# Kernel tuning notes

Hardware: AMD Instinct MI355X
Metric: run time of the kernel (lower is better)

Reference implementation:

```python
import jax, jax.numpy as jnp
import numpy as np

DIM = 1024
HEADS = 16
HEAD_DIM = DIM // HEADS
HIDDEN = 4096
EPS = 1e-5


def _layer_norm(x, w, b):
    mu = jnp.mean(x, axis=-1, keepdims=True)
    var = jnp.var(x, axis=-1, keepdims=True)
    return (x - mu) * jax.lax.rsqrt(var + EPS) * w + b


def setup_inputs() -> dict:
    key = jax.random.key(0)
    ks = jax.random.split(key, 16)
    s = lambda fan_in: 1.0 / np.sqrt(fan_in)
    return {
        "x": jax.random.normal(ks[0], (8, 1024, DIM), dtype=jnp.float32),
        "ln1_w": jnp.ones((DIM,), jnp.float32),
        "ln1_b": jnp.zeros((DIM,), jnp.float32),
        "qkv_w": jax.random.uniform(ks[1], (3 * DIM, DIM), jnp.float32, -s(DIM), s(DIM)),
        "qkv_b": jax.random.uniform(ks[2], (3 * DIM,), jnp.float32, -s(DIM), s(DIM)),
        "out_w": jax.random.uniform(ks[3], (DIM, DIM), jnp.float32, -s(DIM), s(DIM)),
        "out_b": jax.random.uniform(ks[4], (DIM,), jnp.float32, -s(DIM), s(DIM)),
        "ln2_w": jnp.ones((DIM,), jnp.float32),
        "ln2_b": jnp.zeros((DIM,), jnp.float32),
        "fc1_w": jax.random.uniform(ks[5], (HIDDEN, DIM), jnp.float32, -s(DIM), s(DIM)),
        "fc1_b": jax.random.uniform(ks[6], (HIDDEN,), jnp.float32, -s(DIM), s(DIM)),
        "fc2_w": jax.random.uniform(ks[7], (DIM, HIDDEN), jnp.float32, -s(HIDDEN), s(HIDDEN)),
        "fc2_b": jax.random.uniform(ks[8], (DIM,), jnp.float32, -s(HIDDEN), s(HIDDEN)),
    }


def reference(x, ln1_w, ln1_b, qkv_w, qkv_b, out_w, out_b,
              ln2_w, ln2_b, fc1_w, fc1_b, fc2_w, fc2_b):
    B, S, D = x.shape
    # --- attention sub-block (pre-LN) ---
    h = _layer_norm(x, ln1_w, ln1_b)
    qkv = h @ qkv_w.T + qkv_b                              # [B,S,3D]
    qkv = qkv.reshape(B, S, 3, HEADS, HEAD_DIM)
    q, k, v = qkv[:, :, 0], qkv[:, :, 1], qkv[:, :, 2]     # [B,S,H,hd]
    scores = jnp.einsum('bqhd,bkhd->bhqk', q, k) / np.sqrt(HEAD_DIM)
    attn = jax.nn.softmax(scores, axis=-1)
    o = jnp.einsum('bhqk,bkhd->bqhd', attn, v).reshape(B, S, D)
    x = x + (o @ out_w.T + out_b)
    # --- MLP sub-block (pre-LN) ---
    h = _layer_norm(x, ln2_w, ln2_b)
    h = jax.nn.gelu(h @ fc1_w.T + fc1_b, approximate=False)
    x = x + (h @ fc2_w.T + fc2_b)
    return x
```

## Files before the change

### kernel.cpp

```cpp
#include <hip/hip_runtime.h>
#include <hip/hip_bf16.h>

typedef unsigned short u16;
typedef __bf16 bf16x8 __attribute__((ext_vector_type(8)));
typedef float f32x4 __attribute__((ext_vector_type(4)));
typedef u16 u16x8 __attribute__((ext_vector_type(8)));
typedef unsigned u32x2 __attribute__((ext_vector_type(2)));

#define LOG2E 1.4426950408889634f
#define QSCALE 0.18033688011112042f

__device__ __forceinline__ float fast_exp2(float x) {
#if __has_builtin(__builtin_amdgcn_exp2f)
  return __builtin_amdgcn_exp2f(x);
#else
  return exp2f(x);
#endif
}

__device__ __forceinline__ u16 f2bf(float f) {
  union { float f; unsigned u; } c; c.f = f;
  unsigned r = c.u + 0x7fffu + ((c.u >> 16) & 1u);
  return (u16)(r >> 16);
}

__device__ __forceinline__ unsigned pk_bf16(float a, float b) {
#if __has_builtin(__builtin_amdgcn_cvt_pk_bf16_f32)
  typedef __bf16 bf16x2_t __attribute__((ext_vector_type(2)));
  union { bf16x2_t v; unsigned u; } c;
  c.v = __builtin_amdgcn_cvt_pk_bf16_f32(a, b);
  return c.u;
#else
  return (unsigned)f2bf(a) | ((unsigned)f2bf(b) << 16);
#endif
}

__device__ __forceinline__ unsigned pk_bf16_fast(float a, float b) {
#if __has_builtin(__builtin_amdgcn_cvt_pk_bf16_f32)
  return pk_bf16(a, b);
#else
  union { float f; unsigned u; } ca, cb;
  ca.f = a; cb.f = b;
  return __builtin_amdgcn_perm(cb.u, ca.u, 0x07060302u);
#endif
}

__device__ __forceinline__ float gelu_f(float v) {
  float z = 0.7978845608f * v + 0.0356774081f * (v * v * v);
  float e = fast_exp2(z * 2.885390082f);
  float t = 1.0f - 2.0f * __builtin_amdgcn_rcpf(e + 1.0f);
  return 0.5f * v * (1.0f + t);
}

__device__ __forceinline__ void async16(const void* g, void* l) {
  __builtin_amdgcn_global_load_lds(
      (const __attribute__((address_space(1))) void*)g,
      (__attribute__((address_space(3))) void*)l, 16, 0, 0);
}

__global__ __launch_bounds__(256) void cvt4_kernel(
    const float* __restrict__ s0, const float* __restrict__ s1,
    const float* __restrict__ s2, const float* __restrict__ s3,
    u16* __restrict__ d0, u16* __restrict__ d1,
    u16* __restrict__ d2, u16* __restrict__ d3) {
  int i = blockIdx.x * 256 + threadIdx.x;
  const float* s; u16* d; int off;
  if (i < 786432)       { s = s0; d = d0; off = i; }
  else if (i < 1048576) { s = s1; d = d1; off = i - 786432; }
  else if (i < 2097152) { s = s2; d = d2; off = i - 1048576; }
  else                  { s = s3; d = d3; off = i - 2097152; }
  float4 v = ((const float4*)s)[off];
  ushort4 o;
  o.x = f2bf(v.x); o.y = f2bf(v.y); o.z = f2bf(v.z); o.w = f2bf(v.w);
  ((ushort4*)d)[off] = o;
}

__global__ __launch_bounds__(256) void ln_kernel(const float* __restrict__ x,
                                                 const float* __restrict__ w,
                                                 const float* __restrict__ b,
                                                 u16* __restrict__ out) {
  int row = blockIdx.x;
  int tid = threadIdx.x;
  int lane = tid & 63, wave = tid >> 6;
  float4 v = ((const float4*)(x + (size_t)row * 1024))[tid];
  float s = v.x + v.y + v.z + v.w;
  float s2 = v.x*v.x + v.y*v.y + v.z*v.z + v.w*v.w;
  #pragma unroll
  for (int off = 1; off < 64; off <<= 1) {
    s += __shfl_xor(s, off, 64);
    s2 += __shfl_xor(s2, off, 64);
  }
  __shared__ float red[8];
  if (lane == 0) { red[wave] = s; red[4 + wave] = s2; }
  __syncthreads();
  float st = red[0] + red[1] + red[2] + red[3];
  float s2t = red[4] + red[5] + red[6] + red[7];
  float mu = st * (1.0f / 1024.0f);
  float var = s2t * (1.0f / 1024.0f) - mu * mu;
  float rs = rsqrtf(var + 1e-5f);
  float4 wv = ((const float4*)w)[tid];
  float4 bv = ((const float4*)b)[tid];
  ushort4 o;
  o.x = f2bf((v.x - mu) * rs * wv.x + bv.x);
  o.y = f2bf((v.y - mu) * rs * wv.y + bv.y);
  o.z = f2bf((v.z - mu) * rs * wv.z + bv.z);
  o.w = f2bf((v.w - mu) * rs * wv.w + bv.w);
  ((ushort4*)(out + (size_t)row * 1024))[tid] = o;
}

template <int EPI, int TN, int NBLOG2>
__global__ __launch_bounds__(256) void gemm_bt(const u16* __restrict__ A,
                                               const u16* __restrict__ B,
                                               const float* __restrict__ bias,
                                               void* __restrict__ Cout,
                                               const float* __restrict__ resid,
                                               int M, int N, int K) {
  constexpr int NT = TN / 32;
  __shared__ u16 As[128 * 64];
  __shared__ u16 Bs[TN * 64];
  const int tid = threadIdx.x;
  const int lane = tid & 63, wave = tid >> 6;
  const int l15 = lane & 15, l4 = lane >> 4;

  int m0, n0;
  if (NBLOG2 < 0) {
    m0 = blockIdx.y * 128; n0 = blockIdx.x * TN;
  } else {
    const int id = blockIdx.x;
    const int xcd = id & 7;
    const int slot = id >> 3;
    const int ms = slot >> (NBLOG2 < 0 ? 0 : NBLOG2);
    const int nt = slot & ((1 << (NBLOG2 < 0 ? 0 : NBLOG2)) - 1);
    m0 = (ms * 8 + xcd) * 128; n0 = nt * TN;
  }

  const int wr = (wave & 1) * 64, wc = (wave >> 1) * (TN / 2);

  const int srow = lane >> 3;
  const int sg = (lane & 7) ^ (lane >> 3);
  const size_t K8 = (size_t)8 * K;
  const u16* Ag = A + (size_t)(m0 + wave * 32 + srow) * K + sg * 8;
  const u16* Bg = B + (size_t)(n0 + wave * (TN / 4) + srow) * K + sg * 8;
  u16* Al0 = As + wave * 2048;
  u16* Bl0 = Bs + wave * (TN / 4) * 64;
  const int rx = l15 & 7;

  f32x4 acc[4][NT];
  #pragma unroll
  for (int i = 0; i < 4; i++)
    #pragma unroll
    for (int j = 0; j < NT; j++) {
      f32x4 z = {0.f, 0.f, 0.f, 0.f};
      acc[i][j] = z;
    }

  for (int k0 = 0; k0 < K; k0 += 64) {
    __syncthreads();
    #pragma unroll
    for (int t = 0; t < 4; t++) async16(Ag + t * K8 + k0, Al0 + t * 512);
    #pragma unroll
    for (int t = 0; t < NT; t++) async16(Bg + t * K8 + k0, Bl0 + t * 512);
    __syncthreads();
    #pragma unroll
    for (int ks = 0; ks < 2; ks++) {
      const int pg = ((ks * 4 + l4) ^ rx) * 8;
      bf16x8 a[4], b[NT];
      #pragma unroll
      for (int rg = 0; rg < 4; rg++)
        a[rg] = *(const bf16x8*)&As[(wr + rg * 16 + l15) * 64 + pg];
      #pragma unroll
      for (int tg = 0; tg < NT; tg++)
        b[tg] = *(const bf16x8*)&Bs[(wc + tg * 16 + l15) * 64 + pg];
      #pragma unroll
      for (int rg = 0; rg < 4; rg++)
        #pragma unroll
        for (int tg = 0; tg < NT; tg++)
          acc[rg][tg] = __builtin_amdgcn_mfma_f32_16x16x32_bf16(
              a[rg], b[tg], acc[rg][tg], 0, 0, 0);
    }
  }

  float bv[NT];
  #pragma unroll
  for (int tg = 0; tg < NT; tg++) bv[tg] = bias[n0 + wc + tg * 16 + l15];
  #pragma unroll
  for (int rg = 0; rg < 4; rg++) {
    size_t row0 = (size_t)(m0 + wr + rg * 16 + l4 * 4);
    #pragma unroll
    for (int r = 0; r < 4; r += 2) {
      #pragma unroll
      for (int tg = 0; tg < NT; tg++) {
        int col = n0 + wc + tg * 16 + l15;
        float v0 = acc[rg][tg][r] + bv[tg];
        float v1 = acc[rg][tg][r + 1] + bv[tg];
        if (EPI == 1) { v0 = gelu_f(v0); v1 = gelu_f(v1); }
        if (EPI == 3) {
          float sc = (col < 1024) ? QSCALE : 1.0f;
          v0 *= sc; v1 *= sc;
        }
        size_t off0 = (row0 + r) * (size_t)N + col;
        size_t off1 = (row0 + r + 1) * (size_t)N + col;
        if (EPI == 2) {
          ((float*)Cout)[off0] = v0 + resid[off0];
          ((float*)Cout)[off1] = v1 + resid[off1];
        } else {
          unsigned pk = pk_bf16(v0, v1);
          ((u16*)Cout)[off0] = (u16)pk;
          ((u16*)Cout)[off1] = (u16)(pk >> 16);
        }
      }
    }
  }
}

__global__ __launch_bounds__(256) void vtrans_kernel(const u16* __restrict__ qkv,
                                                     u16* __restrict__ vtg) {
  const int sc = blockIdx.x, h = blockIdx.y, b = blockIdx.z;
  const int tid = threadIdx.x;
  __shared__ u16 t[64][72];
  const u16* vp = qkv + ((size_t)b * 1024) * 3072 + h * 64 + 2048;
  #pragma unroll
  for (int it = 0; it < 2; it++) {
    int idx = it * 256 + tid;
    int row = idx >> 3, g = idx & 7;
    *(u16x8*)&t[row][g * 8] =
        *(const u16x8*)(vp + (size_t)(sc * 64 + row) * 3072 + g * 8);
  }
  __syncthreads();
  u16* dst = vtg + ((size_t)(b * 16 + h) * 64) * 1024;
  #pragma unroll
  for (int it = 0; it < 2; it++) {
    int idx = it * 256 + tid;
    int d = idx >> 3, g = idx & 7;
    u16x8 o;
    #pragma unroll
    for (int j = 0; j < 8; j++) o[j] = t[g * 8 + j][d];
    *(u16x8*)(dst + (size_t)d * 1024 + sc * 64 + g * 8) = o;
  }
}

__global__ __launch_bounds__(256) void attn_kernel(const u16* __restrict__ qkv,
                                                   const u16* __restrict__ vtg,
                                                   u16* __restrict__ obuf) {
  const int S = 1024, QKV = 3072;
  const int id = blockIdx.x;
  const int qt = id >> 7, hb = id & 127;
  const int h = hb & 15, b = hb >> 4;
  const int tid = threadIdx.x, lane = tid & 63, wave = tid >> 6;
  const int l15 = lane & 15, l4 = lane >> 4;
  const size_t tok0 = (size_t)b * S;
  const u16* qp = qkv + tok0 * QKV + h * 64;
  const u16* kp = qp + 1024;
  const u16* vtp = vtg + (size_t)(b * 16 + h) * 64 * 1024;
  const int q0 = qt * 128;

  __shared__ u16 Ks[128 * 64];
  __shared__ u16 Vt[64 * 128];
  __shared__ u16 Ps[4][16 * 136];

  const u16* qrow = qp + (size_t)(q0 + wave * 16 + l15) * QKV;
  bf16x8 qf[2][2];
  #pragma unroll
  for (int qs = 0; qs < 2; qs++)
    #pragma unroll
    for (int kb = 0; kb < 2; kb++)
      qf[qs][kb] = *(const bf16x8*)(qrow + (size_t)qs * 64 * QKV + kb * 32 + l4 * 8);

  bf16x8 ones;
  #pragma unroll
  for (int j = 0; j < 8; j++) ones[j] = (__bf16)1.0f;

  const int krow = lane >> 3;
  const int klg = (lane & 7) ^ (lane >> 3);
  const int vrow_i = lane >> 4;
  const int vpg = lane & 15;

  f32x4 oacc[2][4], lacc[2];
  #pragma unroll
  for (int qs = 0; qs < 2; qs++) {
    #pragma unroll
    for (int ct = 0; ct < 4; ct++) {
      f32x4 z = {0.f, 0.f, 0.f, 0.f};
      oacc[qs][ct] = z;
    }
    f32x4 z = {0.f, 0.f, 0.f, 0.f};
    lacc[qs] = z;
  }

  for (int j0 = 0; j0 < S; j0 += 128) {
    __syncthreads();
    #pragma unroll
    for (int t = 0; t < 4; t++) {
      int e = wave * 4 + t;
      async16(kp + (size_t)(j0 + e * 8 + krow) * QKV + klg * 8, Ks + e * 512);
    }
    #pragma unroll
    for (int t = 0; t < 4; t++) {
      int e = wave * 4 + t;
      int row = e * 4 + vrow_i;
      int lg = vpg ^ (row & 15);
      async16(vtp + (size_t)row * 1024 + j0 + lg * 8, Vt + e * 512);
    }
    __syncthreads();

    #pragma unroll
    for (int qs = 0; qs < 2; qs++) {
      f32x4 s[8];
      #pragma unroll
      for (int tg = 0; tg < 8; tg++) {
        f32x4 z = {0.f, 0.f, 0.f, 0.f};
        s[tg] = z;
        #pragma unroll
        for (int kb = 0; kb < 2; kb++) {
          int pg = (kb * 4 + l4) ^ (l15 & 7);
          bf16x8 kf = *(const bf16x8*)&Ks[(tg * 16 + l15) * 64 + pg * 8];
          s[tg] = __builtin_amdgcn_mfma_f32_16x16x32_bf16(kf, qf[qs][kb], s[tg], 0, 0, 0);
        }
      }

      #pragma unroll
      for (int tg = 0; tg < 8; tg++)
        #pragma unroll
        for (int r = 0; r < 4; r++)
          s[tg][r] = fast_exp2(s[tg][r]);

      #pragma unroll
      for (int tg = 0; tg < 8; tg++) {
        u32x2 pr;
        pr[0] = pk_bf16_fast(s[tg][0], s[tg][1]);
        pr[1] = pk_bf16_fast(s[tg][2], s[tg][3]);
        *(u32x2*)&Ps[wave][l15 * 136 + tg * 16 + l4 * 4] = pr;
      }
      bf16x8 pf[4];
      #pragma unroll
      for (int kb = 0; kb < 4; kb++)
        pf[kb] = *(const bf16x8*)&Ps[wave][l15 * 136 + kb * 32 + l4 * 8];

      #pragma unroll
      for (int kb = 0; kb < 4; kb++) {
        #pragma unroll
        for (int ct = 0; ct < 4; ct++) {
          int pg = (kb * 4 + l4) ^ l15;
          bf16x8 vf = *(const bf16x8*)&Vt[(ct * 16 + l15) * 128 + pg * 8];
          oacc[qs][ct] = __builtin_amdgcn_mfma_f32_16x16x32_bf16(
              pf[kb], vf, oacc[qs][ct], 0, 0, 0);
        }
        lacc[qs] = __builtin_amdgcn_mfma_f32_16x16x32_bf16(
            pf[kb], ones, lacc[qs], 0, 0, 0);
      }
    }
  }

  #pragma unroll
  for (int qs = 0; qs < 2; qs++) {
    float inv[4];
    #pragma unroll
    for (int r = 0; r < 4; r++) inv[r] = 1.0f / lacc[qs][r];
    #pragma unroll
    for (int ct = 0; ct < 4; ct++)
      #pragma unroll
      for (int r = 0; r < 4; r++) {
        float v = oacc[qs][ct][r] * inv[r];
        size_t row = tok0 + q0 + qs * 64 + wave * 16 + l4 * 4 + r;
        obuf[row * 1024 + h * 64 + ct * 16 + l15] = f2bf(v);
      }
  }
}

extern "C" void kernel_launch(void* const* d_in, const int* in_sizes, int n_in,
                              void* d_out, int out_size, void* d_ws, size_t ws_size,
                              hipStream_t stream) {
  (void)in_sizes; (void)n_in; (void)out_size; (void)ws_size;
  const float* x     = (const float*)d_in[0];
  const float* ln1_w = (const float*)d_in[1];
  const float* ln1_b = (const float*)d_in[2];
  const float* qkv_w = (const float*)d_in[3];
  const float* qkv_b = (const float*)d_in[4];
  const float* out_w = (const float*)d_in[5];
  const float* out_b = (const float*)d_in[6];
  const float* ln2_w = (const float*)d_in[7];
  const float* ln2_b = (const float*)d_in[8];
  const float* fc1_w = (const float*)d_in[9];
  const float* fc1_b = (const float*)d_in[10];
  const float* fc2_w = (const float*)d_in[11];
  const float* fc2_b = (const float*)d_in[12];
  float* out = (float*)d_out;

  char* ws = (char*)d_ws;
  u16* wqkv = (u16*)(ws);
  u16* wout = (u16*)(ws + 6291456);
  u16* wfc1 = (u16*)(ws + 8388608);
  u16* wfc2 = (u16*)(ws + 16777216);
  u16* hbuf = (u16*)(ws + 25165824);
  u16* qbuf = (u16*)(ws + 41943040);
  u16* vtg  = (u16*)(ws + 92274688);

  const int M = 8192;

  cvt4_kernel<<<dim3(12288), 256, 0, stream>>>(qkv_w, out_w, fc1_w, fc2_w,
                                               wqkv, wout, wfc1, wfc2);

  ln_kernel<<<dim3(M), 256, 0, stream>>>(x, ln1_w, ln1_b, hbuf);
  gemm_bt<3, 128, -1><<<dim3(3072 / 128, M / 128), 256, 0, stream>>>(
      hbuf, wqkv, qkv_b, qbuf, nullptr, M, 3072, 1024);
  vtrans_kernel<<<dim3(16, 16, 8), 256, 0, stream>>>(qbuf, vtg);
  attn_kernel<<<dim3(1024), 256, 0, stream>>>(qbuf, vtg, hbuf);
  gemm_bt<2, 64, -1><<<dim3(1024 / 64, M / 128), 256, 0, stream>>>(
      hbuf, wout, out_b, out, x, M, 1024, 1024);
  ln_kernel<<<dim3(M), 256, 0, stream>>>(out, ln2_w, ln2_b, hbuf);
  gemm_bt<1, 128, -1><<<dim3(4096 / 128, M / 128), 256, 0, stream>>>(
      hbuf, wfc1, fc1_b, qbuf, nullptr, M, 4096, 1024);
  gemm_bt<2, 64, 4><<<dim3((M / 128) * 16), 256, 0, stream>>>(
      qbuf, wfc2, fc2_b, out, out, M, 1024, 4096);
}
```

Before: 502.3 us.

## Replace GEMM kernel with 8-wave double-buffered pipelined MFMA kernel

Replaces the single-buffered 256-thread GEMM with a 512-thread kernel that double-buffers LDS and splits each K-tile into four quadrant phases. Each phase interleaves async global-to-LDS loads for upcoming tiles with MFMA work, using explicit vmcnt waits, barriers, sched_barrier and setprio. Tiles grow to 128x256 or 256x256, which improves operand reuse. The cost is higher register and LDS pressure, and correctness depends on hand-tuned waitcnt counts.

After: 527.6 us. 5.0% more time.

```diff
diff --git a/kernel.cpp b/kernel.cpp
--- a/kernel.cpp
+++ b/kernel.cpp
@@ -9,6 +9,8 @@
 
 #define LOG2E 1.4426950408889634f
 #define QSCALE 0.18033688011112042f
+
+template <int V> struct ic { static constexpr int v = V; };
 
 __device__ __forceinline__ float fast_exp2(float x) {
 #if __has_builtin(__builtin_amdgcn_exp2f)
@@ -57,6 +59,10 @@
       (const __attribute__((address_space(1))) void*)g,
       (__attribute__((address_space(3))) void*)l, 16, 0, 0);
 }
+
+#define CFENCE asm volatile("" ::: "memory")
+#define VMCNT(N) do { asm volatile("s_waitcnt vmcnt(" #N ")" ::: "memory"); \
+                      __builtin_amdgcn_sched_barrier(0); } while (0)
 
 __global__ __launch_bounds__(256) void cvt4_kernel(
     const float* __restrict__ s0, const float* __restrict__ s1,
@@ -108,109 +114,180 @@
   ((ushort4*)(out + (size_t)row * 1024))[tid] = o;
 }
 
-template <int EPI, int TN, int NBLOG2>
-__global__ __launch_bounds__(256) void gemm_bt(const u16* __restrict__ A,
-                                               const u16* __restrict__ B,
-                                               const float* __restrict__ bias,
-                                               void* __restrict__ Cout,
-                                               const float* __restrict__ resid,
-                                               int M, int N, int K) {
-  constexpr int NT = TN / 32;
-  __shared__ u16 As[128 * 64];
-  __shared__ u16 Bs[TN * 64];
+template <int EPI, int BM, int BN, int NBLOG2>
+__global__ __launch_bounds__(512, 2) void gemm8(const u16* __restrict__ A,
+                                                const u16* __restrict__ B,
+                                                const float* __restrict__ bias,
+                                                void* __restrict__ Cout,
+                                                const float* __restrict__ resid,
+                                                int M, int N, int K) {
+  (void)M;
+  constexpr int FMH = BM / 64;
+  constexpr int FNH = BN / 128;
+  constexpr int LA = BM / 128;
+  constexpr int LB = BN / 128;
+  constexpr int STEADY = LA + LB;
+  __shared__ u16 As[2][BM * 64];
+  __shared__ u16 Bs[2][BN * 64];
   const int tid = threadIdx.x;
   const int lane = tid & 63, wave = tid >> 6;
+  const int wr = wave & 1, wc = wave >> 1;
   const int l15 = lane & 15, l4 = lane >> 4;
+  const int nt = K >> 6;
 
   int m0, n0;
-  if (NBLOG2 < 0) {
-    m0 = blockIdx.y * 128; n0 = blockIdx.x * TN;
+  if constexpr (NBLOG2 < 0) {
+    m0 = blockIdx.y * BM; n0 = blockIdx.x * BN;
   } else {
     const int id = blockIdx.x;
-    const int xcd = id & 7;
-    const int slot = id >> 3;
-    const int ms = slot >> (NBLOG2 < 0 ? 0 : NBLOG2);
-    const int nt = slot & ((1 << (NBLOG2 < 0 ? 0 : NBLOG2)) - 1);
-    m0 = (ms * 8 + xcd) * 128; n0 = nt * TN;
-  }
-
-  const int wr = (wave & 1) * 64, wc = (wave >> 1) * (TN / 2);
+    const int xcd = id & 7, slot = id >> 3;
+    m0 = ((slot >> NBLOG2) * 8 + xcd) * BM;
+    n0 = (slot & ((1 << NBLOG2) - 1)) * BN;
+  }
 
   const int srow = lane >> 3;
-  const int sg = (lane & 7) ^ (lane >> 3);
-  const size_t K8 = (size_t)8 * K;
-  const u16* Ag = A + (size_t)(m0 + wave * 32 + srow) * K + sg * 8;
-  const u16* Bg = B + (size_t)(n0 + wave * (TN / 4) + srow) * K + sg * 8;
-  u16* Al0 = As + wave * 2048;
-  u16* Bl0 = Bs + wave * (TN / 4) * 64;
-  const int rx = l15 & 7;
-
-  f32x4 acc[4][NT];
-  #pragma unroll
-  for (int i = 0; i < 4; i++)
-    #pragma unroll
-    for (int j = 0; j < NT; j++) {
-      f32x4 z = {0.f, 0.f, 0.f, 0.f};
-      acc[i][j] = z;
-    }
-
-  for (int k0 = 0; k0 < K; k0 += 64) {
-    __syncthreads();
-    #pragma unroll
-    for (int t = 0; t < 4; t++) async16(Ag + t * K8 + k0, Al0 + t * 512);
-    #pragma unroll
-    for (int t = 0; t < NT; t++) async16(Bg + t * K8 + k0, Bl0 + t * 512);
-    __syncthreads();
-    #pragma unroll
-    for (int ks = 0; ks < 2; ks++) {
-      const int pg = ((ks * 4 + l4) ^ rx) * 8;
-      bf16x8 a[4], b[NT];
-      #pragma unroll
-      for (int rg = 0; rg < 4; rg++)
-        a[rg] = *(const bf16x8*)&As[(wr + rg * 16 + l15) * 64 + pg];
-      #pragma unroll
-      for (int tg = 0; tg < NT; tg++)
-        b[tg] = *(const bf16x8*)&Bs[(wc + tg * 16 + l15) * 64 + pg];
-      #pragma unroll
-      for (int rg = 0; rg < 4; rg++)
-        #pragma unroll
-        for (int tg = 0; tg < NT; tg++)
-          acc[rg][tg] = __builtin_amdgcn_mfma_f32_16x16x32_bf16(
-              a[rg], b[tg], acc[rg][tg], 0, 0, 0);
-    }
-  }
-
-  float bv[NT];
-  #pragma unroll
-  for (int tg = 0; tg < NT; tg++) bv[tg] = bias[n0 + wc + tg * 16 + l15];
-  #pragma unroll
-  for (int rg = 0; rg < 4; rg++) {
-    size_t row0 = (size_t)(m0 + wr + rg * 16 + l4 * 4);
-    #pragma unroll
-    for (int r = 0; r < 4; r += 2) {
-      #pragma unroll
-      for (int tg = 0; tg < NT; tg++) {
-        int col = n0 + wc + tg * 16 + l15;
-        float v0 = acc[rg][tg][r] + bv[tg];
-        float v1 = acc[rg][tg][r + 1] + bv[tg];
-        if (EPI == 1) { v0 = gelu_f(v0); v1 = gelu_f(v1); }
-        if (EPI == 3) {
-          float sc = (col < 1024) ? QSCALE : 1.0f;
-          v0 *= sc; v1 *= sc;
+  const int sg = (lane & 7) ^ srow;
+  const u16* Ab = A + (size_t)(m0 + srow) * K + sg * 8;
+  const u16* Bb = B + (size_t)(n0 + srow) * K + sg * 8;
+
+  auto stageA = [&](int tile, int half, int wb) {
+    if (tile >= nt) return;
+    #pragma unroll
+    for (int t = 0; t < LA; t++) {
+      const int r0 = half * (BM / 2) + wave * (BM / 16) + t * 8;
+      async16(Ab + (size_t)r0 * K + tile * 64, &As[wb][r0 * 64]);
+    }
+  };
+  auto stageB = [&](int tile, int half, int wb) {
+    if (tile >= nt) return;
+    #pragma unroll
+    for (int t = 0; t < LB; t++) {
+      const int r0 = half * (BN / 2) + wave * (BN / 16) + t * 8;
+      async16(Bb + (size_t)r0 * K + tile * 64, &Bs[wb][r0 * 64]);
+    }
+  };
+
+  f32x4 acc[2][FMH][2][FNH];
+  #pragma unroll
+  for (int a = 0; a < 2; a++)
+    #pragma unroll
+    for (int f = 0; f < FMH; f++)
+      #pragma unroll
+      for (int c = 0; c < 2; c++)
+        #pragma unroll
+        for (int g = 0; g < FNH; g++) {
+          f32x4 z = {0.f, 0.f, 0.f, 0.f};
+          acc[a][f][c][g] = z;
         }
-        size_t off0 = (row0 + r) * (size_t)N + col;
-        size_t off1 = (row0 + r + 1) * (size_t)N + col;
-        if (EPI == 2) {
-          ((float*)Cout)[off0] = v0 + resid[off0];
-          ((float*)Cout)[off1] = v1 + resid[off1];
-        } else {
-          unsigned pk = pk_bf16(v0, v1);
-          ((u16*)Cout)[off0] = (u16)pk;
-          ((u16*)Cout)[off1] = (u16)(pk >> 16);
-        }
-      }
-    }
-  }
+
+  auto phase = [&](auto qa_, auto qb_, int rb, auto stage) {
+    constexpr int qa = decltype(qa_)::v;
+    constexpr int qb = decltype(qb_)::v;
+    bf16x8 af[FMH][2], bfr[FNH][2];
+    #pragma unroll
+    for (int f = 0; f < FMH; f++)
+      #pragma unroll
+      for (int ks = 0; ks < 2; ks++) {
+        const int row = qa * (BM / 2) + wr * (BM / 4) + f * 16 + l15;
+        const int sl = (ks * 4 + l4) ^ (l15 & 7);
+        af[f][ks] = *(const bf16x8*)&As[rb][row * 64 + sl * 8];
+      }
+    #pragma unroll
+    for (int f = 0; f < FNH; f++)
+      #pragma unroll
+      for (int ks = 0; ks < 2; ks++) {
+        const int col = qb * (BN / 2) + wc * (BN / 8) + f * 16 + l15;
+        const int sl = (ks * 4 + l4) ^ (l15 & 7);
+        bfr[f][ks] = *(const bf16x8*)&Bs[rb][col * 64 + sl * 8];
+      }
+    stage();
+    CFENCE;
+    __builtin_amdgcn_s_barrier();
+    asm volatile("s_waitcnt lgkmcnt(0)" ::: "memory");
+    __builtin_amdgcn_sched_barrier(0);
+    __builtin_amdgcn_s_setprio(1);
+    #pragma unroll
+    for (int f = 0; f < FMH; f++)
+      #pragma unroll
+      for (int g = 0; g < FNH; g++)
+        #pragma unroll
+        for (int ks = 0; ks < 2; ks++)
+          acc[qa][f][qb][g] = __builtin_amdgcn_mfma_f32_16x16x32_bf16(
+              af[f][ks], bfr[g][ks], acc[qa][f][qb][g], 0, 0, 0);
+    __builtin_amdgcn_s_setprio(0);
+    __builtin_amdgcn_sched_barrier(0);
+  };
+
+  auto endphase = [&](int mode) {
+    if (mode == 1) {
+      if constexpr (STEADY == 4) VMCNT(4); else VMCNT(3);
+    } else if (mode == 2) {
+      VMCNT(0);
+    }
+    CFENCE;
+    __builtin_amdgcn_s_barrier();
+  };
+
+  stageA(0, 0, 0); stageB(0, 0, 0); stageA(0, 1, 0); stageB(0, 1, 0);
+  stageA(1, 0, 1); stageB(1, 0, 1);
+  if constexpr (STEADY == 4) VMCNT(4); else VMCNT(3);
+  CFENCE;
+  __builtin_amdgcn_s_barrier();
+
+  const int niter = nt >> 1;
+  for (int it = 0; it < niter; ++it) {
+    const int T = 2 * it;
+    const int f4 = (T + 2 < nt) ? 1 : 2;
+    const int f8 = (T + 3 < nt) ? 1 : 2;
+    phase(ic<0>{}, ic<0>{}, 0, [&]{ stageA(T + 1, 1, 1); }); endphase(0);
+    phase(ic<0>{}, ic<1>{}, 0, [&]{ stageB(T + 1, 1, 1); }); endphase(0);
+    phase(ic<1>{}, ic<0>{}, 0, [&]{ stageA(T + 2, 0, 0); }); endphase(0);
+    phase(ic<1>{}, ic<1>{}, 0, [&]{ stageB(T + 2, 0, 0); }); endphase(f4);
+    phase(ic<0>{}, ic<0>{}, 1, [&]{ stageA(T + 2, 1, 0); }); endphase(0);
+    phase(ic<0>{}, ic<1>{}, 1, [&]{ stageB(T + 2, 1, 0); }); endphase(0);
+    phase(ic<1>{}, ic<0>{}, 1, [&]{ stageA(T + 3, 0, 1); }); endphase(0);
+    phase(ic<1>{}, ic<1>{}, 1, [&]{ stageB(T + 3, 0, 1); }); endphase(f8);
+  }
+
+  float bv[2][FNH];
+  #pragma unroll
+  for (int qb = 0; qb < 2; qb++)
+    #pragma unroll
+    for (int fn = 0; fn < FNH; fn++)
+      bv[qb][fn] = bias[n0 + qb * (BN / 2) + wc * (BN / 8) + fn * 16 + l15];
+
+  #pragma unroll
+  for (int qa = 0; qa < 2; qa++)
+    #pragma unroll
+    for (int fm = 0; fm < FMH; fm++) {
+      const size_t row0 =
+          (size_t)(m0 + qa * (BM / 2) + wr * (BM / 4) + fm * 16 + l4 * 4);
+      #pragma unroll
+      for (int r = 0; r < 4; r += 2)
+        #pragma unroll
+        for (int qb = 0; qb < 2; qb++)
+          #pragma unroll
+          for (int fn = 0; fn < FNH; fn++) {
+            const int col = n0 + qb * (BN / 2) + wc * (BN / 8) + fn * 16 + l15;
+            float v0 = acc[qa][fm][qb][fn][r] + bv[qb][fn];
+            float v1 = acc[qa][fm][qb][fn][r + 1] + bv[qb][fn];
+            if (EPI == 1) { v0 = gelu_f(v0); v1 = gelu_f(v1); }
+            if (EPI == 3) {
+              float sc = (col < 1024) ? QSCALE : 1.0f;
+              v0 *= sc; v1 *= sc;
+            }
+            const size_t off0 = (row0 + r) * (size_t)N + col;
+            const size_t off1 = (row0 + r + 1) * (size_t)N + col;
+            if (EPI == 2) {
+              ((float*)Cout)[off0] = v0 + resid[off0];
+              ((float*)Cout)[off1] = v1 + resid[off1];
+            } else {
+              unsigned pk = pk_bf16(v0, v1);
+              ((u16*)Cout)[off0] = (u16)pk;
+              ((u16*)Cout)[off1] = (u16)(pk >> 16);
+            }
+          }
+    }
 }
 
 __global__ __launch_bounds__(256) void vtrans_kernel(const u16* __restrict__ qkv,
@@ -401,15 +478,15 @@
                                                wqkv, wout, wfc1, wfc2);
 
   ln_kernel<<<dim3(M), 256, 0, stream>>>(x, ln1_w, ln1_b, hbuf);
-  gemm_bt<3, 128, -1><<<dim3(3072 / 128, M / 128), 256, 0, stream>>>(
+  gemm8<3, 128, 256, -1><<<dim3(3072 / 256, M / 128), 512, 0, stream>>>(
       hbuf, wqkv, qkv_b, qbuf, nullptr, M, 3072, 1024);
   vtrans_kernel<<<dim3(16, 16, 8), 256, 0, stream>>>(qbuf, vtg);
   attn_kernel<<<dim3(1024), 256, 0, stream>>>(qbuf, vtg, hbuf);
-  gemm_bt<2, 64, -1><<<dim3(1024 / 64, M / 128), 256, 0, stream>>>(
+  gemm8<2, 128, 256, -1><<<dim3(1024 / 256, M / 128), 512, 0, stream>>>(
       hbuf, wout, out_b, out, x, M, 1024, 1024);
   ln_kernel<<<dim3(M), 256, 0, stream>>>(out, ln2_w, ln2_b, hbuf);
-  gemm_bt<1, 128, -1><<<dim3(4096 / 128, M / 128), 256, 0, stream>>>(
+  gemm8<1, 256, 256, -1><<<dim3(4096 / 256, M / 256), 512, 0, stream>>>(
       hbuf, wfc1, fc1_b, qbuf, nullptr, M, 4096, 1024);
-  gemm_bt<2, 64, 4><<<dim3((M / 128) * 16), 256, 0, stream>>>(
+  gemm8<2, 128, 256, 2><<<dim3((M / 128) * (1024 / 256)), 512, 0, stream>>>(
       qbuf, wfc2, fc2_b, out, out, M, 1024, 4096);
 }
```
